# Kernel optimization log

Hardware: AMD Instinct MI355X
Metric: run time of the kernel (lower is better)

## Reference

```python
import jax, jax.numpy as jnp
import numpy as np

F = 26  # num_sparse_features
B, D = 16384, 128

# upper-triangular indices over the (F+1)x(F+1) interaction matrix, offset=1
_IU0, _IU1 = np.triu_indices(F + 1, k=1)
_IU0 = jnp.asarray(_IU0)
_IU1 = jnp.asarray(_IU1)


def setup_inputs() -> dict:
    key = jax.random.key(0)
    k1, k2 = jax.random.split(key)
    dense_features = jax.random.normal(k1, (B, D), dtype=jnp.float32)
    sparse_features = jax.random.normal(k2, (B, F, D), dtype=jnp.float32)
    return {"dense_features": dense_features, "sparse_features": sparse_features}


def reference(dense_features, sparse_features):
    # combined: [B, F+1, D]
    combined = jnp.concatenate([dense_features[:, None, :], sparse_features], axis=1)
    # pairwise dot products: [B, F+1, F+1]
    interactions = jnp.einsum("bfd,bgd->bfg", combined, combined)
    # gather strict upper triangle: [B, (F+1)*F/2]
    interactions_flat = interactions[:, _IU0, _IU1]
    # output: [B, D + (F+1)*F/2]
    return jnp.concatenate([dense_features, interactions_flat], axis=1)
```

## Files before the change

kernel.cpp:

```cpp
#include <hip/hip_runtime.h>


#define DD 128
#define FF 26
#define OUTW 479

typedef _Float16 half8_t __attribute__((ext_vector_type(8)));
typedef float f32x4 __attribute__((ext_vector_type(4)));

__device__ __forceinline__ half8_t cvt8(f32x4 x, f32x4 y) {
  half8_t h;
  h[0] = (_Float16)x[0]; h[1] = (_Float16)x[1];
  h[2] = (_Float16)x[2]; h[3] = (_Float16)x[3];
  h[4] = (_Float16)y[0]; h[5] = (_Float16)y[1];
  h[6] = (_Float16)y[2]; h[7] = (_Float16)y[3];
  return h;
}

__global__ __launch_bounds__(256) void dlrm_interact(
    const float* __restrict__ dense,
    const float* __restrict__ sparse,
    float* __restrict__ out, int Btot) {
  const int wave = threadIdx.x >> 6;
  const int lane = threadIdx.x & 63;
  const int b = blockIdx.x * 4 + wave;
  if (b >= Btot) return;

  const int col  = lane & 15;
  const int quad = lane >> 4;
  const int koff = quad * 8;

  const int f0 = col;
  int f1 = 16 + col; if (f1 > 26) f1 = 26;

  const float* row0 = (f0 == 0)
      ? (dense + (size_t)b * DD)
      : (sparse + ((size_t)b * FF + (f0 - 1)) * DD);
  const float* row1 = sparse + ((size_t)b * FF + (f1 - 1)) * DD;

  f32x4 a0[4][2], a1[4][2];
#pragma unroll
  for (int ks = 0; ks < 4; ++ks) {
    const int k = ks * 32 + koff;
    a0[ks][0] = *(const f32x4*)(row0 + k);
    a0[ks][1] = *(const f32x4*)(row0 + k + 4);
    a1[ks][0] = *(const f32x4*)(row1 + k);
    a1[ks][1] = *(const f32x4*)(row1 + k + 4);
  }

  f32x4 c00 = {0.f, 0.f, 0.f, 0.f};
  f32x4 c01 = {0.f, 0.f, 0.f, 0.f};
  f32x4 c11 = {0.f, 0.f, 0.f, 0.f};
#pragma unroll
  for (int ks = 0; ks < 4; ++ks) {
    half8_t v0 = cvt8(a0[ks][0], a0[ks][1]);
    half8_t v1 = cvt8(a1[ks][0], a1[ks][1]);
    c00 = __builtin_amdgcn_mfma_f32_16x16x32_f16(v0, v0, c00, 0, 0, 0);
    c01 = __builtin_amdgcn_mfma_f32_16x16x32_f16(v0, v1, c01, 0, 0, 0);
    c11 = __builtin_amdgcn_mfma_f32_16x16x32_f16(v1, v1, c11, 0, 0, 0);
  }

  float* orow = out + (size_t)b * OUTW;

  const float* drow = dense + (size_t)b * DD;
  orow[2 * lane]     = drow[2 * lane];
  orow[2 * lane + 1] = drow[2 * lane + 1];

  float* oint = orow + DD;
#pragma unroll
  for (int r = 0; r < 4; ++r) {
    const int i = quad * 4 + r;
    const int j = col;
    if (i < j) oint[i * (53 - i) / 2 + (j - i - 1)] = c00[r];
  }
#pragma unroll
  for (int r = 0; r < 4; ++r) {
    const int i = quad * 4 + r;
    const int j = 16 + col;
    if (j <= 26) oint[i * (53 - i) / 2 + (j - i - 1)] = c01[r];
  }
#pragma unroll
  for (int r = 0; r < 4; ++r) {
    const int i = 16 + quad * 4 + r;
    const int j = 16 + col;
    if (i < j && j <= 26) oint[i * (53 - i) / 2 + (j - i - 1)] = c11[r];
  }
}

extern "C" void kernel_launch(void* const* d_in, const int* in_sizes, int n_in,
                              void* d_out, int out_size, void* d_ws, size_t ws_size,
                              hipStream_t stream) {
  const float* dense  = (const float*)d_in[0];
  const float* sparse = (const float*)d_in[1];
  float* out = (float*)d_out;
  const int Btot = in_sizes[0] / DD;
  const int grid = (Btot + 3) / 4;
  hipLaunchKernelGGL(dlrm_interact, dim3(grid), dim3(256), 0, stream,
                     dense, sparse, out, Btot);
}
```

Baseline: 311.0 us.

## Stage inputs and outputs through LDS for coalesced global loads and stores

Each block now loads its four batch rows of sparse and dense features with fully coalesced 16-byte loads, converts them to fp16, and writes them into padded shared memory. The MFMA operands are then read from LDS. Results go to an LDS output buffer and are written to global memory contiguously across the block. This replaces scattered per-lane global reads and stores with coalesced streaming, at the cost of extra LDS traffic, two barriers, and dropping the tail bounds check, so the batch size must be a multiple of 4.

```diff
diff --git a/kernel.cpp b/kernel.cpp
--- a/kernel.cpp
+++ b/kernel.cpp
@@ -1,89 +1,105 @@
 #include <hip/hip_runtime.h>
 
 
-#define DD 128
-#define FF 26
+#define DD   128
+#define FF   26
 #define OUTW 479
+#define PD   136
+#define NR   27
+#define RS   (NR * PD)
+#define OS   480
 
 typedef _Float16 half8_t __attribute__((ext_vector_type(8)));
+typedef _Float16 half4_t __attribute__((ext_vector_type(4)));
 typedef float f32x4 __attribute__((ext_vector_type(4)));
-
-__device__ __forceinline__ half8_t cvt8(f32x4 x, f32x4 y) {
-  half8_t h;
-  h[0] = (_Float16)x[0]; h[1] = (_Float16)x[1];
-  h[2] = (_Float16)x[2]; h[3] = (_Float16)x[3];
-  h[4] = (_Float16)y[0]; h[5] = (_Float16)y[1];
-  h[6] = (_Float16)y[2]; h[7] = (_Float16)y[3];
-  return h;
-}
 
 __global__ __launch_bounds__(256) void dlrm_interact(
     const float* __restrict__ dense,
     const float* __restrict__ sparse,
-    float* __restrict__ out, int Btot) {
-  const int wave = threadIdx.x >> 6;
-  const int lane = threadIdx.x & 63;
-  const int b = blockIdx.x * 4 + wave;
-  if (b >= Btot) return;
+    float* __restrict__ out) {
+  __shared__ _Float16 Xs[4 * RS];
+  __shared__ float    Os[4 * OS];
+
+  const int t    = threadIdx.x;
+  const int wave = t >> 6;
+  const int lane = t & 63;
+  const int b0   = blockIdx.x * 4;
+
+  const float* sp = sparse + (size_t)b0 * (FF * DD);
+  f32x4 v[13];
+#pragma unroll
+  for (int it = 0; it < 13; ++it)
+    v[it] = *(const f32x4*)(sp + (size_t)(t + it * 256) * 4);
+
+  f32x4 dv;
+  if (t < 128) dv = *(const f32x4*)(dense + (size_t)b0 * DD + t * 4);
+
+#pragma unroll
+  for (int it = 0; it < 13; ++it) {
+    const int c   = t + it * 256;
+    const int i   = c * 4;
+    const int r   = i / (FF * DD);
+    const int rem = i - r * (FF * DD);
+    const int f   = rem >> 7;
+    const int k   = rem & 127;
+    half4_t h;
+    h[0] = (_Float16)v[it][0]; h[1] = (_Float16)v[it][1];
+    h[2] = (_Float16)v[it][2]; h[3] = (_Float16)v[it][3];
+    *(half4_t*)&Xs[r * RS + (f + 1) * PD + k] = h;
+  }
+  if (t < 128) {
+    const int r = t >> 5;
+    const int k = (t & 31) * 4;
+    half4_t h;
+    h[0] = (_Float16)dv[0]; h[1] = (_Float16)dv[1];
+    h[2] = (_Float16)dv[2]; h[3] = (_Float16)dv[3];
+    *(half4_t*)&Xs[r * RS + k] = h;
+    *(f32x4*)&Os[r * OS + k]   = dv;
+  }
+  __syncthreads();
 
   const int col  = lane & 15;
   const int quad = lane >> 4;
-  const int koff = quad * 8;
+  const _Float16* xr = &Xs[wave * RS];
+  const int f1 = (16 + col > 26) ? 26 : (16 + col);
 
-  const int f0 = col;
-  int f1 = 16 + col; if (f1 > 26) f1 = 26;
-
-  const float* row0 = (f0 == 0)
-      ? (dense + (size_t)b * DD)
-      : (sparse + ((size_t)b * FF + (f0 - 1)) * DD);
-  const float* row1 = sparse + ((size_t)b * FF + (f1 - 1)) * DD;
-
-  f32x4 a0[4][2], a1[4][2];
+  f32x4 c00 = {0.f,0.f,0.f,0.f}, c01 = {0.f,0.f,0.f,0.f}, c11 = {0.f,0.f,0.f,0.f};
 #pragma unroll
   for (int ks = 0; ks < 4; ++ks) {
-    const int k = ks * 32 + koff;
-    a0[ks][0] = *(const f32x4*)(row0 + k);
-    a0[ks][1] = *(const f32x4*)(row0 + k + 4);
-    a1[ks][0] = *(const f32x4*)(row1 + k);
-    a1[ks][1] = *(const f32x4*)(row1 + k + 4);
-  }
-
-  f32x4 c00 = {0.f, 0.f, 0.f, 0.f};
-  f32x4 c01 = {0.f, 0.f, 0.f, 0.f};
-  f32x4 c11 = {0.f, 0.f, 0.f, 0.f};
-#pragma unroll
-  for (int ks = 0; ks < 4; ++ks) {
-    half8_t v0 = cvt8(a0[ks][0], a0[ks][1]);
-    half8_t v1 = cvt8(a1[ks][0], a1[ks][1]);
+    half8_t v0 = *(const half8_t*)(xr + col * PD + ks * 32 + quad * 8);
+    half8_t v1 = *(const half8_t*)(xr + f1  * PD + ks * 32 + quad * 8);
     c00 = __builtin_amdgcn_mfma_f32_16x16x32_f16(v0, v0, c00, 0, 0, 0);
     c01 = __builtin_amdgcn_mfma_f32_16x16x32_f16(v0, v1, c01, 0, 0, 0);
     c11 = __builtin_amdgcn_mfma_f32_16x16x32_f16(v1, v1, c11, 0, 0, 0);
   }
 
-  float* orow = out + (size_t)b * OUTW;
-
-  const float* drow = dense + (size_t)b * DD;
-  orow[2 * lane]     = drow[2 * lane];
-  orow[2 * lane + 1] = drow[2 * lane + 1];
-
-  float* oint = orow + DD;
+  float* oi = &Os[wave * OS + DD];
 #pragma unroll
   for (int r = 0; r < 4; ++r) {
-    const int i = quad * 4 + r;
-    const int j = col;
-    if (i < j) oint[i * (53 - i) / 2 + (j - i - 1)] = c00[r];
+    const int i = quad * 4 + r, j = col;
+    if (i < j) oi[i * (53 - i) / 2 + (j - i - 1)] = c00[r];
   }
 #pragma unroll
   for (int r = 0; r < 4; ++r) {
-    const int i = quad * 4 + r;
-    const int j = 16 + col;
-    if (j <= 26) oint[i * (53 - i) / 2 + (j - i - 1)] = c01[r];
+    const int i = quad * 4 + r, j = 16 + col;
+    if (j <= 26) oi[i * (53 - i) / 2 + (j - i - 1)] = c01[r];
   }
 #pragma unroll
   for (int r = 0; r < 4; ++r) {
-    const int i = 16 + quad * 4 + r;
-    const int j = 16 + col;
-    if (i < j && j <= 26) oint[i * (53 - i) / 2 + (j - i - 1)] = c11[r];
+    const int i = 16 + quad * 4 + r, j = 16 + col;
+    if (i < j && j <= 26) oi[i * (53 - i) / 2 + (j - i - 1)] = c11[r];
+  }
+  __syncthreads();
+
+  float* og = out + (size_t)b0 * OUTW;
+#pragma unroll
+  for (int it = 0; it < 8; ++it) {
+    const int j = t + it * 256;
+    if (j < 4 * OUTW) {
+      const int r = j / OUTW;
+      const int k = j - r * OUTW;
+      og[j] = Os[r * OS + k];
+    }
   }
 }
 
@@ -94,7 +110,7 @@
   const float* sparse = (const float*)d_in[1];
   float* out = (float*)d_out;
   const int Btot = in_sizes[0] / DD;
-  const int grid = (Btot + 3) / 4;
+  const int grid = Btot / 4;
   hipLaunchKernelGGL(dlrm_interact, dim3(grid), dim3(256), 0, stream,
-                     dense, sparse, out, Btot);
+                     dense, sparse, out);
 }
```

New measurement: 308.8 us. No clear change (-0.7%).
